# Kernel optimization log

Measured on AMD Instinct MI355X. Metric: run time of the kernel, lower is better.

The kernel has to match this reference:

```python
import jax, jax.numpy as jnp
import numpy as np
import math

N_FEATURES = 64
GAMMA_ORDER = 0.5
ALPHA, BETA, ETA = 0.3, 0.4, 0.3
MAX_K = 50


def _make_coeffs():
    # gamma_values[0] = Gamma(g+1); gamma_values[m] (m>=1) = Gamma(m)*Gamma(g-m+2)
    g0 = math.gamma(GAMMA_ORDER + 1.0)
    coeffs = np.zeros(MAX_K + 1, dtype=np.float32)
    coeffs[0] = 1.0
    for k in range(1, MAX_K + 1):
        gv_k = math.gamma(k) * math.gamma(GAMMA_ORDER - k + 2.0)
        coeffs[k] = ((-1.0) ** k) * g0 / gv_k
    return jnp.asarray(coeffs)


def setup_inputs() -> dict:
    key = jax.random.key(0)
    k1, k2, k3, k4 = jax.random.split(key, 4)
    B, T, F = 4, 8192, N_FEATURES
    x = jax.random.normal(k1, (B, T, F), dtype=jnp.float32)
    weight_matrix = jax.random.normal(k2, (F, F), dtype=jnp.float32)
    bound = 1.0 / math.sqrt(F)
    proj_w = jax.random.uniform(k3, (F, F), dtype=jnp.float32, minval=-bound, maxval=bound)
    proj_b = jax.random.uniform(k4, (F,), dtype=jnp.float32, minval=-bound, maxval=bound)
    kappa = jnp.float32(0.1)
    coeffs = _make_coeffs()
    return {"x": x, "weight_matrix": weight_matrix, "proj_w": proj_w,
            "proj_b": proj_b, "kappa": kappa, "coeffs": coeffs}


def _fractional_derivative(x, coeffs):
    # causal conv: result[:, t, :] = sum_{k=0}^{min(t, max_k)} coeffs[k] * x[:, t-k, :]
    K = coeffs.shape[0]
    F = x.shape[-1]
    # depthwise 1D cross-correlation; kernel reversed so it implements x[t-k]
    kern = jnp.tile(coeffs[::-1][:, None, None], (1, 1, F))  # [K, 1, F]
    return jax.lax.conv_general_dilated(
        x, kern, window_strides=(1,), padding=[(K - 1, 0)],
        dimension_numbers=("NWC", "WIO", "NWC"), feature_group_count=F)


def reference(x, weight_matrix, proj_w, proj_b, kappa, coeffs):
    B, T, F = x.shape
    # 1) memory term: fractional derivative (causal conv)
    memory_term = _fractional_derivative(x, coeffs)

    # 2) coupling term: sum_j w[i,j] * tanh(x_i - x_j) * sigmoid(|x_i| + |x_j|)
    #    diagonal contributes tanh(0)=0, matching the i != j skip in the original.
    w = jax.nn.softmax(weight_matrix, axis=1)                 # [F, F]
    xi = x[..., :, None]                                      # [B, T, F, 1]
    xj = x[..., None, :]                                      # [B, T, 1, F]
    c = jnp.tanh(xi - xj) * jax.nn.sigmoid(jnp.abs(xi) + jnp.abs(xj))  # [B,T,F,F]
    coupling_term = jnp.einsum("btij,ij->bti", c, w)

    # 3) global term: proj(x[:, t]) * sum_{s=0}^{t} exp(-kappa * s)
    proj = x @ proj_w.T + proj_b                               # [B, T, F]
    kernel_cumsum = jnp.cumsum(jnp.exp(-kappa * jnp.arange(T, dtype=x.dtype)))
    global_term = proj * kernel_cumsum[None, :, None]

    output = ALPHA * memory_term + BETA * coupling_term + ETA * global_term
    return (output, memory_term)
```

## Files before the change

kernel.cpp:

```cpp
#include <hip/hip_runtime.h>
#include <hip/hip_fp16.h>
#include <math.h>

#define TT 8192
#define FF 64
#define TILE 64
#define HALO 50
#define ROWS 114
#define XSTR 72

typedef float f32x2 __attribute__((ext_vector_type(2)));
typedef float f32x4 __attribute__((ext_vector_type(4)));
typedef _Float16 f16x8 __attribute__((ext_vector_type(8)));
typedef unsigned int u32x4 __attribute__((ext_vector_type(4)));
typedef unsigned int u32x2 __attribute__((ext_vector_type(2)));

__device__ __forceinline__ float rcpf(float x) { return __builtin_amdgcn_rcpf(x); }

__global__ void prep_kernel(const float* __restrict__ W, const float* __restrict__ PW,
                            const float* __restrict__ C,
                            __half* __restrict__ wsmH, u32x4* __restrict__ pwB,
                            float* __restrict__ cpad2) {
    const int lane = threadIdx.x;
    const int wv   = threadIdx.y;
    const int tid  = wv * 64 + lane;
    for (int it = 0; it < 16; ++it) {
        const int r = wv * 16 + it;
        float v = W[r * 64 + lane];
        float m = v;
        #pragma unroll
        for (int off = 32; off >= 1; off >>= 1)
            m = fmaxf(m, __shfl_xor(m, off, 64));
        float e = __expf(v - m);
        float s = e;
        #pragma unroll
        for (int off = 32; off >= 1; off >>= 1)
            s += __shfl_xor(s, off, 64);
        wsmH[lane * 64 + r] = __float2half(e * rcpf(s));
    }
    for (int s = tid; s < 512; s += 256) {
        const int n2 = s >> 6;
        const int ln = s & 63;
        const int i  = (n2 >> 1) * 16 + (ln & 15);
        const int k0 = (n2 & 1) * 32 + (ln >> 4) * 8;
        u32x4 frag;
        #pragma unroll
        for (int w = 0; w < 4; ++w) {
            const unsigned lo = __half_as_ushort(__float2half_rn(PW[i * 64 + k0 + 2 * w]));
            const unsigned hi = __half_as_ushort(__float2half_rn(PW[i * 64 + k0 + 2 * w + 1]));
            frag[w] = lo | (hi << 16);
        }
        pwB[s] = frag;
    }
    if (tid < 65) {
        const int k = tid - 7;
        cpad2[tid] = (k >= 0 && k <= 50) ? C[k] : 0.f;
    }
}

__global__ __launch_bounds__(512, 4)
void mcao_main(const float* __restrict__ x,
               const __half* __restrict__ wsmH,
               const u32x4* __restrict__ pwB,
               const float* __restrict__ cpad2,
               const float* __restrict__ pb,
               const float* __restrict__ kap,
               float* __restrict__ out,
               float* __restrict__ memout) {
    __shared__ __align__(16) char smem[57888];
    __half* xsH = (__half*)smem;
    f32x2*  tuS = (f32x2*)(smem + 16416);
    float*  P2  = (float*)(smem + 16416);
    __half* wT  = (__half*)(smem + 49696);

    const int tid  = threadIdx.x;
    const int lane = tid & 63;
    const int wv   = tid >> 6;

    const int sw = ((int)blockIdx.x & 7) * 64 + ((int)blockIdx.x >> 3);
    const int b  = sw >> 7;
    const int t0 = (sw & 127) * TILE;
    const float* xb = x + (size_t)b * TT * FF;

    for (int i4 = tid; i4 < ROWS * 16; i4 += 512) {
        const int s = i4 >> 4, f4 = i4 & 15, t = t0 - HALO + s;
        f32x4 v = {0.f, 0.f, 0.f, 0.f};
        if (t >= 0) v = *(const f32x4*)(xb + (size_t)t * 64 + f4 * 4);
        __half hv[4];
        #pragma unroll
        for (int q = 0; q < 4; ++q) hv[q] = __float2half_rn(v[q]);
        *(u32x2*)(&xsH[s * XSTR + f4 * 4]) = *(u32x2*)hv;
        if (s >= HALO) {
            const int row = s - HALO;
            #pragma unroll
            for (int q = 0; q < 4; ++q) {
                f32x2 e;
                e.x = fmaf(-2.f, rcpf(__expf(2.f * v[q]) + 1.f), 1.f);
                e.y = __expf(-fabsf(v[q]));
                tuS[(f4 * 4 + q) * 65 + row] = e;
            }
        }
    }
    ((f32x4*)wT)[tid] = ((const f32x4*)wsmH)[tid];
    __syncthreads();

    const int mt = wv >> 1;
    const int marow = HALO + mt * 16 + (lane & 15);
    const int kcol  = (lane >> 4) * 8;
    f32x4 cfr[2] = {{0.f,0.f,0.f,0.f}, {0.f,0.f,0.f,0.f}};
    #pragma unroll
    for (int tb = 0; tb < 2; ++tb) {
        const int nt = (wv & 1) * 2 + tb;
        #pragma unroll
        for (int kt = 0; kt < 2; ++kt) {
            const f16x8 afr = *(const f16x8*)(&xsH[marow * XSTR + kt * 32 + kcol]);
            const f16x8 bfr = __builtin_bit_cast(f16x8, pwB[(nt * 2 + kt) * 64 + lane]);
            cfr[tb] = __builtin_amdgcn_mfma_f32_16x16x32_f16(afr, bfr, cfr[tb], 0, 0, 0);
        }
    }

    const int r  = lane;
    const int ib = wv * 8;
    f32x2 tiP[4], uiP[4];
    #pragma unroll
    for (int q = 0; q < 8; ++q) {
        const f32x2 e = tuS[(ib + q) * 65 + r];
        tiP[q >> 1][q & 1] = e.x;
        uiP[q >> 1][q & 1] = e.y;
    }

    float macc[8] = {0,0,0,0,0,0,0,0};
    f32x2 cac[4] = {{0,0},{0,0},{0,0},{0,0}};
    const f32x2 one2 = {1.f, 1.f};
    const int firrow = 8 * wv;

    #pragma unroll
    for (int m = 0; m < 64; ++m) {
        const f32x2 e = tuS[m * 65 + r];
        __half wh[8];
        *(u32x4*)wh = *(const u32x4*)(&wT[m * 64 + ib]);
        if (m < 58) {
            const float xv = __half2float(xsH[(firrow + m) * XSTR + lane]);
            #pragma unroll
            for (int r2 = 0; r2 < 8; ++r2)
                macc[r2] = fmaf(cpad2[r2 + 57 - m], xv, macc[r2]);
        }
        const f32x2 tjj = {e.x, e.x}, ujj = {e.y, e.y};
        #pragma unroll
        for (int g = 0; g < 4; ++g) {
            const f32x2 d1  = __builtin_elementwise_fma(-tiP[g], tjj, one2);
            const f32x2 d2  = __builtin_elementwise_fma( uiP[g], ujj, one2);
            const f32x2 den = d1 * d2;
            f32x2 rr; rr.x = rcpf(den.x); rr.y = rcpf(den.y);
            const f32x2 s = (tiP[g] - tjj) * rr;
            cac[g].x = fmaf(__half2float(wh[2*g]),   s.x, cac[g].x);
            cac[g].y = fmaf(__half2float(wh[2*g+1]), s.y, cac[g].y);
        }
    }

    #pragma unroll
    for (int r2 = 0; r2 < 8; ++r2)
        memout[(size_t)(b * TT + t0 + firrow + r2) * 64 + lane] = macc[r2];

    __syncthreads();

    #pragma unroll
    for (int tb = 0; tb < 2; ++tb) {
        const int nt = (wv & 1) * 2 + tb;
        const int ic = nt * 16 + (lane & 15);
        const int rb = mt * 16 + (lane >> 4) * 4;
        #pragma unroll
        for (int reg = 0; reg < 4; ++reg)
            P2[ic * 65 + rb + reg] = cfr[tb][reg];
    }
    __syncthreads();

    const float kappa = kap[0];
    const float ksum  = (1.f - __expf(-kappa * (float)(t0 + r + 1))) *
                        rcpf(1.f - __expf(-kappa));
    #pragma unroll
    for (int q = 0; q < 8; ++q) {
        const float cv  = (q & 1) ? cac[q >> 1].y : cac[q >> 1].x;
        const int   idx = (ib + q) * 65 + r;
        P2[idx] = fmaf(0.4f, cv, 0.3f * (P2[idx] + pb[ib + q]) * ksum);
    }
    __syncthreads();

    #pragma unroll
    for (int rr2 = 0; rr2 < 8; ++rr2) {
        const int row = firrow + rr2;
        out[(size_t)(b * TT + t0 + row) * 64 + lane] =
            fmaf(0.3f, macc[rr2], P2[lane * 65 + row]);
    }
}

extern "C" void kernel_launch(void* const* d_in, const int* in_sizes, int n_in,
                              void* d_out, int out_size, void* d_ws, size_t ws_size,
                              hipStream_t stream) {
    const float* x   = (const float*)d_in[0];
    const float* W   = (const float*)d_in[1];
    const float* PW  = (const float*)d_in[2];
    const float* pb  = (const float*)d_in[3];
    const float* kap = (const float*)d_in[4];
    const float* cf  = (const float*)d_in[5];

    float* out    = (float*)d_out;
    float* memout = out + (size_t)4 * TT * FF;

    __half* wsmH  = (__half*)d_ws;
    u32x4*  pwB   = (u32x4*)((char*)d_ws + 8192);
    float*  cpad2 = (float*)((char*)d_ws + 16384);

    hipLaunchKernelGGL(prep_kernel, dim3(1), dim3(64, 4), 0, stream,
                       W, PW, cf, wsmH, pwB, cpad2);
    hipLaunchKernelGGL(mcao_main, dim3(4 * (TT / TILE)), dim3(512), 0, stream,
                       x, wsmH, pwB, cpad2, pb, kap, out, memout);
}
```

Before: 43.90 us.

## Exploit antisymmetry of coupling term to halve pairwise tanh-sigmoid evaluations

The pairwise coupling term c(i,j) is antisymmetric (tanh odd, sigmoid symmetric), so each unordered feature pair is now evaluated once. The result is accumulated into row i with w[i,j] and subtracted from row j with w[j,i], using both a transposed and a normal fp32 softmax matrix read from global memory. Off-block contributions go through LDS atomicAdd into a zeroed accumulator, and the memory FIR is moved ahead of the loop. This roughly halves the rcp-heavy pairwise ALU work. In exchange it adds LDS atomics, extra global weight loads and some work imbalance between waves.

Measured after the change: 61.24 us. +39.5%, slower.

```diff
diff --git a/kernel.cpp b/kernel.cpp
--- a/kernel.cpp
+++ b/kernel.cpp
@@ -19,8 +19,8 @@
 
 __global__ void prep_kernel(const float* __restrict__ W, const float* __restrict__ PW,
                             const float* __restrict__ C,
-                            __half* __restrict__ wsmH, u32x4* __restrict__ pwB,
-                            float* __restrict__ cpad2) {
+                            float* __restrict__ wsmT, float* __restrict__ wsmN,
+                            u32x4* __restrict__ pwB, float* __restrict__ cpad2) {
     const int lane = threadIdx.x;
     const int wv   = threadIdx.y;
     const int tid  = wv * 64 + lane;
@@ -36,7 +36,9 @@
         #pragma unroll
         for (int off = 32; off >= 1; off >>= 1)
             s += __shfl_xor(s, off, 64);
-        wsmH[lane * 64 + r] = __float2half(e * rcpf(s));
+        const float w = e * rcpf(s);
+        wsmT[lane * 64 + r] = w;
+        wsmN[r * 64 + lane] = w;
     }
     for (int s = tid; s < 512; s += 256) {
         const int n2 = s >> 6;
@@ -60,7 +62,8 @@
 
 __global__ __launch_bounds__(512, 4)
 void mcao_main(const float* __restrict__ x,
-               const __half* __restrict__ wsmH,
+               const float* __restrict__ wsmT,
+               const float* __restrict__ wsmN,
                const u32x4* __restrict__ pwB,
                const float* __restrict__ cpad2,
                const float* __restrict__ pb,
@@ -68,10 +71,11 @@
                float* __restrict__ out,
                float* __restrict__ memout) {
     __shared__ __align__(16) char smem[57888];
-    __half* xsH = (__half*)smem;
-    f32x2*  tuS = (f32x2*)(smem + 16416);
-    float*  P2  = (float*)(smem + 16416);
-    __half* wT  = (__half*)(smem + 49696);
+    __half* xsH  = (__half*)smem;
+    float*  tS   = (float*)(smem + 16416);
+    float*  P2   = (float*)(smem + 16416);
+    __half* uH   = (__half*)(smem + 33056);
+    float*  Pacc = (float*)(smem + 41504);
 
     const int tid  = threadIdx.x;
     const int lane = tid & 63;
@@ -81,6 +85,8 @@
     const int b  = sw >> 7;
     const int t0 = (sw & 127) * TILE;
     const float* xb = x + (size_t)b * TT * FF;
+
+    for (int i = tid; i < 64 * 64; i += 512) Pacc[i] = 0.f;
 
     for (int i4 = tid; i4 < ROWS * 16; i4 += 512) {
         const int s = i4 >> 4, f4 = i4 & 15, t = t0 - HALO + s;
@@ -94,15 +100,26 @@
             const int row = s - HALO;
             #pragma unroll
             for (int q = 0; q < 4; ++q) {
-                f32x2 e;
-                e.x = fmaf(-2.f, rcpf(__expf(2.f * v[q]) + 1.f), 1.f);
-                e.y = __expf(-fabsf(v[q]));
-                tuS[(f4 * 4 + q) * 65 + row] = e;
+                const int f = f4 * 4 + q;
+                tS[f * 65 + row] = fmaf(-2.f, rcpf(__expf(2.f * v[q]) + 1.f), 1.f);
+                uH[f * 66 + row] = __float2half(__expf(-fabsf(v[q])));
             }
         }
     }
-    ((f32x4*)wT)[tid] = ((const f32x4*)wsmH)[tid];
-    __syncthreads();
+    __syncthreads();
+
+    const int firrow = 8 * wv;
+    float macc[8] = {0,0,0,0,0,0,0,0};
+    #pragma unroll
+    for (int m = 0; m < 58; ++m) {
+        const float xv = __half2float(xsH[(firrow + m) * XSTR + lane]);
+        #pragma unroll
+        for (int r2 = 0; r2 < 8; ++r2)
+            macc[r2] = fmaf(cpad2[r2 + 57 - m], xv, macc[r2]);
+    }
+    #pragma unroll
+    for (int r2 = 0; r2 < 8; ++r2)
+        memout[(size_t)(b * TT + t0 + firrow + r2) * 64 + lane] = macc[r2];
 
     const int mt = wv >> 1;
     const int marow = HALO + mt * 16 + (lane & 15);
@@ -120,49 +137,75 @@
     }
 
     const int r  = lane;
-    const int ib = wv * 8;
-    f32x2 tiP[4], uiP[4];
+    const int I8 = __builtin_amdgcn_readfirstlane(wv * 8);
+    float tA[8], uA[8];
     #pragma unroll
     for (int q = 0; q < 8; ++q) {
-        const f32x2 e = tuS[(ib + q) * 65 + r];
-        tiP[q >> 1][q & 1] = e.x;
-        uiP[q >> 1][q & 1] = e.y;
-    }
-
-    float macc[8] = {0,0,0,0,0,0,0,0};
-    f32x2 cac[4] = {{0,0},{0,0},{0,0},{0,0}};
-    const f32x2 one2 = {1.f, 1.f};
-    const int firrow = 8 * wv;
-
-    #pragma unroll
-    for (int m = 0; m < 64; ++m) {
-        const f32x2 e = tuS[m * 65 + r];
-        __half wh[8];
-        *(u32x4*)wh = *(const u32x4*)(&wT[m * 64 + ib]);
-        if (m < 58) {
-            const float xv = __half2float(xsH[(firrow + m) * XSTR + lane]);
+        tA[q] = tS[(I8 + q) * 65 + r];
+        uA[q] = __half2float(uH[(I8 + q) * 66 + r]);
+    }
+    float accI[8] = {0,0,0,0,0,0,0,0};
+
+    #pragma unroll
+    for (int bq = 1; bq < 8; ++bq) {
+        const int gb = I8 + bq;
+        const f32x4 wT0 = *(const f32x4*)(wsmT + gb * 64 + I8);
+        const f32x4 wT1 = *(const f32x4*)(wsmT + gb * 64 + I8 + 4);
+        const f32x4 wN0 = *(const f32x4*)(wsmN + gb * 64 + I8);
+        const f32x4 wN1 = *(const f32x4*)(wsmN + gb * 64 + I8 + 4);
+        float accJ = 0.f;
+        #pragma unroll
+        for (int a = 0; a < 8; ++a) {
+            if (a < bq) {
+                const float d1 = fmaf(-tA[a], tA[bq], 1.f);
+                const float d2 = fmaf( uA[a], uA[bq], 1.f);
+                const float rr = rcpf(d1 * d2);
+                const float s  = (tA[a] - tA[bq]) * rr;
+                const float wT = (a < 4) ? wT0[a] : wT1[a - 4];
+                const float wN = (a < 4) ? wN0[a] : wN1[a - 4];
+                accI[a] = fmaf(wT, s, accI[a]);
+                accJ    = fmaf(wN, s, accJ);
+            }
+        }
+        accI[bq] -= accJ;
+    }
+
+    #pragma unroll
+    for (int d = 1; d <= 4; ++d) {
+        if (d < 4 || wv < 4) {
+            const int J8 = __builtin_amdgcn_readfirstlane(((wv + d) & 7) * 8);
             #pragma unroll
-            for (int r2 = 0; r2 < 8; ++r2)
-                macc[r2] = fmaf(cpad2[r2 + 57 - m], xv, macc[r2]);
-        }
-        const f32x2 tjj = {e.x, e.x}, ujj = {e.y, e.y};
-        #pragma unroll
-        for (int g = 0; g < 4; ++g) {
-            const f32x2 d1  = __builtin_elementwise_fma(-tiP[g], tjj, one2);
-            const f32x2 d2  = __builtin_elementwise_fma( uiP[g], ujj, one2);
-            const f32x2 den = d1 * d2;
-            f32x2 rr; rr.x = rcpf(den.x); rr.y = rcpf(den.y);
-            const f32x2 s = (tiP[g] - tjj) * rr;
-            cac[g].x = fmaf(__half2float(wh[2*g]),   s.x, cac[g].x);
-            cac[g].y = fmaf(__half2float(wh[2*g+1]), s.y, cac[g].y);
-        }
-    }
-
-    #pragma unroll
-    for (int r2 = 0; r2 < 8; ++r2)
-        memout[(size_t)(b * TT + t0 + firrow + r2) * 64 + lane] = macc[r2];
-
-    __syncthreads();
+            for (int bb = 0; bb < 8; ++bb) {
+                const int gb = J8 + bb;
+                const float tb2 = tS[gb * 65 + r];
+                const float ub2 = __half2float(uH[gb * 66 + r]);
+                const f32x4 wT0 = *(const f32x4*)(wsmT + gb * 64 + I8);
+                const f32x4 wT1 = *(const f32x4*)(wsmT + gb * 64 + I8 + 4);
+                const f32x4 wN0 = *(const f32x4*)(wsmN + gb * 64 + I8);
+                const f32x4 wN1 = *(const f32x4*)(wsmN + gb * 64 + I8 + 4);
+                float accJ = 0.f;
+                #pragma unroll
+                for (int a = 0; a < 8; ++a) {
+                    const float d1 = fmaf(-tA[a], tb2, 1.f);
+                    const float d2 = fmaf( uA[a], ub2, 1.f);
+                    const float rr = rcpf(d1 * d2);
+                    const float s  = (tA[a] - tb2) * rr;
+                    const float wT = (a < 4) ? wT0[a] : wT1[a - 4];
+                    const float wN = (a < 4) ? wN0[a] : wN1[a - 4];
+                    accI[a] = fmaf(wT, s, accI[a]);
+                    accJ    = fmaf(wN, s, accJ);
+                }
+                atomicAdd(&Pacc[gb * 64 + r], -accJ);
+            }
+        }
+    }
+
+    __syncthreads();
+
+    float cc[8];
+    #pragma unroll
+    for (int q = 0; q < 8; ++q)
+        cc[q] = accI[q] + Pacc[(I8 + q) * 64 + r];
 
     #pragma unroll
     for (int tb = 0; tb < 2; ++tb) {
@@ -180,9 +223,8 @@
                         rcpf(1.f - __expf(-kappa));
     #pragma unroll
     for (int q = 0; q < 8; ++q) {
-        const float cv  = (q & 1) ? cac[q >> 1].y : cac[q >> 1].x;
-        const int   idx = (ib + q) * 65 + r;
-        P2[idx] = fmaf(0.4f, cv, 0.3f * (P2[idx] + pb[ib + q]) * ksum);
+        const int idx = (I8 + q) * 65 + r;
+        P2[idx] = fmaf(0.4f, cc[q], 0.3f * (P2[idx] + pb[I8 + q]) * ksum);
     }
     __syncthreads();
 
@@ -207,12 +249,13 @@
     float* out    = (float*)d_out;
     float* memout = out + (size_t)4 * TT * FF;
 
-    __half* wsmH  = (__half*)d_ws;
-    u32x4*  pwB   = (u32x4*)((char*)d_ws + 8192);
-    float*  cpad2 = (float*)((char*)d_ws + 16384);
+    float*  wsmT  = (float*)d_ws;
+    float*  wsmN  = (float*)((char*)d_ws + 16384);
+    u32x4*  pwB   = (u32x4*)((char*)d_ws + 32768);
+    float*  cpad2 = (float*)((char*)d_ws + 40960);
 
     hipLaunchKernelGGL(prep_kernel, dim3(1), dim3(64, 4), 0, stream,
-                       W, PW, cf, wsmH, pwB, cpad2);
+                       W, PW, cf, wsmT, wsmN, pwB, cpad2);
     hipLaunchKernelGGL(mcao_main, dim3(4 * (TT / TILE)), dim3(512), 0, stream,
-                       x, wsmH, pwB, cpad2, pb, kap, out, memout);
+                       x, wsmT, wsmN, pwB, cpad2, pb, kap, out, memout);
 }
```
